# Optimization experiments

Measured on AMD Instinct MI355X. Metric: run time of the kernel, lower is better.

The kernel has to match this reference:

```python
import jax, jax.numpy as jnp
import numpy as np

D_MODEL = 1024
NUM_HEADS = 16
D_K = D_MODEL // NUM_HEADS
THETA = 10000.0
BATCH, SEQ = 2, 2048


def apply_rope(x, token_positions, theta):
    # x: [..., heads, seq, d_k]; interleaved pair rotation
    d = x.shape[-1]
    inv_freq = theta ** (-jnp.arange(0, d, 2, dtype=jnp.float32) / d)  # [d/2]
    ang = token_positions.astype(jnp.float32)[:, None] * inv_freq[None, :]  # [seq, d/2]
    cos, sin = jnp.cos(ang), jnp.sin(ang)  # broadcast over batch/heads
    x_even = x[..., 0::2]
    x_odd = x[..., 1::2]
    out_even = x_even * cos - x_odd * sin
    out_odd = x_even * sin + x_odd * cos
    out = jnp.stack([out_even, out_odd], axis=-1)  # [..., seq, d/2, 2]
    return out.reshape(x.shape)


def setup_inputs() -> dict:
    key = jax.random.key(0)
    ks = jax.random.split(key, 5)
    scale = 1.0 / np.sqrt(D_MODEL)
    return {
        "x": jax.random.normal(ks[0], (BATCH, SEQ, D_MODEL), dtype=jnp.float32),
        "wq": jax.random.normal(ks[1], (D_MODEL, D_MODEL), dtype=jnp.float32) * scale,
        "wk": jax.random.normal(ks[2], (D_MODEL, D_MODEL), dtype=jnp.float32) * scale,
        "wv": jax.random.normal(ks[3], (D_MODEL, D_MODEL), dtype=jnp.float32) * scale,
        "wo": jax.random.normal(ks[4], (D_MODEL, D_MODEL), dtype=jnp.float32) * scale,
        "token_positions": jnp.arange(SEQ, dtype=jnp.int32),
    }


def reference(x, wq, wk, wv, wo, token_positions):
    B, S, _ = x.shape
    # fused-style QKV projections: weight layout is [d_out, d_in]
    xq = jnp.einsum("bsd,kd->bsk", x, wq)
    xk = jnp.einsum("bsd,kd->bsk", x, wk)
    xv = jnp.einsum("bsd,vd->bsv", x, wv)
    # split heads: [b, h, s, d_h]
    def split(t):
        return t.reshape(B, S, NUM_HEADS, D_K).transpose(0, 2, 1, 3)
    xq, xk, xv = split(xq), split(xk), split(xv)
    xq = apply_rope(xq, token_positions, THETA)
    xk = apply_rope(xk, token_positions, THETA)
    scores = jnp.einsum("bhqd,bhkd->bhqk", xq, xk) / jnp.sqrt(jnp.float32(D_K))
    causal = jnp.tril(jnp.ones((S, S), dtype=bool))
    scores = jnp.where(causal, scores, -jnp.inf)
    attn = jax.nn.softmax(scores, axis=-1)
    out = jnp.einsum("bhqk,bhkd->bhqd", attn, xv)
    out = out.transpose(0, 2, 1, 3).reshape(B, S, D_MODEL)  # merge heads
    return jnp.einsum("bsv,dv->bsd", out, wo)
```

## Files before the change

### kernel.cpp

```cpp
#include <hip/hip_runtime.h>

typedef __attribute__((ext_vector_type(8))) short short8;
typedef __attribute__((ext_vector_type(4))) short short4v;
typedef __attribute__((ext_vector_type(4))) float floatx4;

__device__ inline ushort f2b(float f) {
    union { uint i; float f; } c; c.f = f;
    uint i = c.i;
    uint r = (i + 0x7FFFu + ((i >> 16) & 1u)) >> 16;
    return (ushort)r;
}

__device__ __forceinline__ void load_lds16(const ushort* g, ushort* l) {
    __builtin_amdgcn_global_load_lds((const __attribute__((address_space(1))) void*)g,
                                     (__attribute__((address_space(3))) void*)l, 16, 0, 0);
}

__global__ __launch_bounds__(256) void cvt4_k(const float* __restrict__ x,
                                              const float* __restrict__ wq,
                                              const float* __restrict__ wk,
                                              const float* __restrict__ wv,
                                              ushort* __restrict__ xb,
                                              ushort* __restrict__ wqb,
                                              ushort* __restrict__ wkb,
                                              ushort* __restrict__ wvb,
                                              const int* __restrict__ pos,
                                              float2* __restrict__ tab) {
    const int blk = blockIdx.x;
    if (blk >= 3584) {
        const int idx = (blk - 3584) * 256 + threadIdx.x;
        const int s = idx >> 5, fi = idx & 31;
        const float inv = exp2f(-(float)fi * 0.41524101186092557f);
        const float ang = (float)pos[s] * inv;
        float sn, cs;
        sincosf(ang, &sn, &cs);
        tab[idx] = make_float2(cs, sn);
        return;
    }
    const float* in; ushort* out; int base;
    if (blk < 2048)      { in = x;  out = xb;  base = blk; }
    else if (blk < 2560) { in = wq; out = wqb; base = blk - 2048; }
    else if (blk < 3072) { in = wk; out = wkb; base = blk - 2560; }
    else                 { in = wv; out = wvb; base = blk - 3072; }
    const int i = (base * 256 + threadIdx.x) * 8;
    float4 f0 = *(const float4*)(in + i);
    float4 f1 = *(const float4*)(in + i + 4);
    ushort u[8] = {f2b(f0.x), f2b(f0.y), f2b(f0.z), f2b(f0.w),
                   f2b(f1.x), f2b(f1.y), f2b(f1.z), f2b(f1.w)};
    *(uint4*)(out + i) = *(const uint4*)u;
}

template <bool OUTF32, bool BF32>
__device__ __forceinline__ void gemm_body(ushort* As, ushort* Bs,
                                          const ushort* __restrict__ A,
                                          const ushort* __restrict__ Bb,
                                          const float* __restrict__ B32,
                                          void* __restrict__ C,
                                          int N, int m0, int n0,
                                          bool doRope, const float2* __restrict__ tab,
                                          float oscale) {
    const int tid = threadIdx.x;
    const int wave = tid >> 6, lane = tid & 63;
    const int quad = lane >> 4, l16 = lane & 15;
    const int wm = (wave >> 1) * 64, wn = (wave & 1) * 64;

    floatx4 acc[4][4] = {};

    const int cA = tid, cB = tid + 256;
    const int rA = cA >> 2, jgA = ((cA & 3) - (rA >> 1)) & 3;
    const int rB = cB >> 2, jgB = ((cB & 3) - (rB >> 1)) & 3;
    const ushort* gaA = A + (size_t)(m0 + rA) * 1024 + jgA * 8;
    const ushort* gaB = A + (size_t)(m0 + rB) * 1024 + jgB * 8;
    const ushort* gbA = nullptr;
    const ushort* gbB = nullptr;
    const float*  hbA = nullptr;
    const float*  hbB = nullptr;
    if constexpr (!BF32) {
        gbA = Bb + (size_t)(n0 + rA) * 1024 + jgA * 8;
        gbB = Bb + (size_t)(n0 + rB) * 1024 + jgB * 8;
    } else {
        hbA = B32 + (size_t)(n0 + rA) * 1024 + jgA * 8;
        hbB = B32 + (size_t)(n0 + rB) * 1024 + jgB * 8;
    }

    load_lds16(gaA, As + cA * 8);
    load_lds16(gaB, As + cB * 8);
    if constexpr (!BF32) {
        load_lds16(gbA, Bs + cA * 8);
        load_lds16(gbB, Bs + cB * 8);
    } else {
        float4 a0 = *(const float4*)hbA, a1 = *(const float4*)(hbA + 4);
        float4 b0 = *(const float4*)hbB, b1 = *(const float4*)(hbB + 4);
        ushort ua[8] = {f2b(a0.x), f2b(a0.y), f2b(a0.z), f2b(a0.w),
                        f2b(a1.x), f2b(a1.y), f2b(a1.z), f2b(a1.w)};
        ushort ub[8] = {f2b(b0.x), f2b(b0.y), f2b(b0.z), f2b(b0.w),
                        f2b(b1.x), f2b(b1.y), f2b(b1.z), f2b(b1.w)};
        *(uint4*)(Bs + cA * 8) = *(const uint4*)ua;
        *(uint4*)(Bs + cB * 8) = *(const uint4*)ub;
    }
    __syncthreads();

    for (int kt = 0; kt < 32; ++kt) {
        const int cur = kt & 1;
        const int nb = (cur ^ 1) * 4096;
        float4 pa0, pa1, pb0, pb1;
        if (kt + 1 < 32) {
            load_lds16(gaA + (kt + 1) * 32, As + nb + cA * 8);
            load_lds16(gaB + (kt + 1) * 32, As + nb + cB * 8);
            if constexpr (!BF32) {
                load_lds16(gbA + (kt + 1) * 32, Bs + nb + cA * 8);
                load_lds16(gbB + (kt + 1) * 32, Bs + nb + cB * 8);
            } else {
                const float* pA = hbA + (kt + 1) * 32;
                const float* pB = hbB + (kt + 1) * 32;
                pa0 = *(const float4*)pA; pa1 = *(const float4*)(pA + 4);
                pb0 = *(const float4*)pB; pb1 = *(const float4*)(pB + 4);
            }
        }
        const ushort* as = As + cur * 4096;
        const ushort* bs = Bs + cur * 4096;
        short8 af[4], bf[4];
#pragma unroll
        for (int i = 0; i < 4; ++i) {
            const int ra = wm + i * 16 + l16;
            const int rb = wn + i * 16 + l16;
            af[i] = *(const short8*)(as + ra * 32 + (((quad + (ra >> 1)) & 3) << 3));
            bf[i] = *(const short8*)(bs + rb * 32 + (((quad + (rb >> 1)) & 3) << 3));
        }
#pragma unroll
        for (int mi = 0; mi < 4; ++mi)
#pragma unroll
            for (int ni = 0; ni < 4; ++ni)
                acc[mi][ni] = __builtin_amdgcn_mfma_f32_16x16x32_bf16(af[mi], bf[ni], acc[mi][ni], 0, 0, 0);
        if constexpr (BF32) {
            if (kt + 1 < 32) {
                ushort ua[8] = {f2b(pa0.x), f2b(pa0.y), f2b(pa0.z), f2b(pa0.w),
                                f2b(pa1.x), f2b(pa1.y), f2b(pa1.z), f2b(pa1.w)};
                ushort ub[8] = {f2b(pb0.x), f2b(pb0.y), f2b(pb0.z), f2b(pb0.w),
                                f2b(pb1.x), f2b(pb1.y), f2b(pb1.z), f2b(pb1.w)};
                *(uint4*)(Bs + nb + cA * 8) = *(const uint4*)ua;
                *(uint4*)(Bs + nb + cB * 8) = *(const uint4*)ub;
            }
        }
        __syncthreads();
    }
#pragma unroll
    for (int mi = 0; mi < 4; ++mi) {
        const int row = m0 + wm + mi * 16 + quad * 4;
#pragma unroll
        for (int ni = 0; ni < 4; ++ni) {
            const int col = n0 + wn + ni * 16 + l16;
            const int fi = ((wn + ni * 16 + l16) & 63) >> 1;
#pragma unroll
            for (int r = 0; r < 4; ++r) {
                float v = acc[mi][ni][r];
                if (doRope) {
                    const float other = __shfl_xor(v, 1);
                    const float2 cs = tab[((row + r) & 2047) * 32 + fi];
                    v = (col & 1) ? (other * cs.y + v * cs.x) : (v * cs.x - other * cs.y);
                }
                v *= oscale;
                if (OUTF32) ((float*)C)[(size_t)(row + r) * N + col] = v;
                else        ((ushort*)C)[(size_t)(row + r) * N + col] = f2b(v);
            }
        }
    }
}

__global__ __launch_bounds__(256) void gemm_qkv(const ushort* __restrict__ xb,
                                                const ushort* __restrict__ wqb,
                                                const ushort* __restrict__ wkb,
                                                const ushort* __restrict__ wvb,
                                                ushort* __restrict__ q,
                                                ushort* __restrict__ k,
                                                ushort* __restrict__ vt,
                                                const float2* __restrict__ tab) {
    __shared__ __align__(16) ushort As[8192], Bs[8192];
    const int blk = blockIdx.x;
    const int swz = (blk & 7) * 96 + (blk >> 3);
    const int job = swz >> 8, r = swz & 255;
    const ushort *A, *B;
    ushort* C;
    int N, m0, n0;
    bool rope;
    float osc;
    if (job == 0)      { A = xb;  B = wqb; C = q;  N = 1024; m0 = (r >> 3) * 128; n0 = (r & 7) * 128; rope = true;  osc = 0.18033688011112042f; }
    else if (job == 1) { A = xb;  B = wkb; C = k;  N = 1024; m0 = (r >> 3) * 128; n0 = (r & 7) * 128; rope = true;  osc = 1.0f; }
    else               { A = wvb; B = xb;  C = vt; N = 4096; m0 = (r & 7) * 128;  n0 = (r >> 3) * 128; rope = false; osc = 1.0f; }
    gemm_body<false, false>(As, Bs, A, B, nullptr, C, N, m0, n0, rope, tab, osc);
}

__global__ __launch_bounds__(256) void gemm_o(const ushort* __restrict__ A,
                                              const float* __restrict__ wo,
                                              float* __restrict__ C) {
    __shared__ __align__(16) ushort As[8192], Bs[8192];
    const int blk = blockIdx.x;
    const int swz = (blk & 7) * 32 + (blk >> 3);
    const int m = swz >> 3, n = swz & 7;
    gemm_body<true, true>(As, Bs, A, nullptr, wo, C, 1024, m * 128, n * 128, false, nullptr, 1.0f);
}

__global__ __launch_bounds__(256, 4) void attn_k(const ushort* __restrict__ Qg,
                                                 const ushort* __restrict__ Kg,
                                                 const ushort* __restrict__ Vtg,
                                                 ushort* __restrict__ Og) {
    __shared__ __align__(16) ushort Ks[2][4096];
    __shared__ __align__(16) ushort Vs[2][4096];

    const int tid = threadIdx.x;
    const int wave = tid >> 6, lane = tid & 63;
    const int quad = lane >> 4, l16 = lane & 15;
    const int blk = blockIdx.x;
    const int bh = blk & 31;
    const int qt = 31 - (blk >> 5);
    const int b = bh >> 4, h = bh & 15;
    const int bq = b * 2048;
    const int wl = wave * 16 + l16;
    const int nk = qt + 1, dt = nk - 1;

    const int cA = tid, cB = tid + 256;
    const int sA = cA >> 3, jA = ((cA & 7) - sA) & 7;
    const int sB = cB >> 3, jB = ((cB & 7) - sB) & 7;
    const ushort* kgA = Kg + (size_t)(bq + sA) * 1024 + h * 64 + jA * 8;
    const ushort* kgB = Kg + (size_t)(bq + sB) * 1024 + h * 64 + jB * 8;
    const ushort* vgA = Vtg + (size_t)(h * 64 + sA) * 4096 + bq + jA * 8;
    const ushort* vgB = Vtg + (size_t)(h * 64 + sB) * 4096 + bq + jB * 8;

    const int kb0 = l16 * 64 + (((quad + l16) & 7) << 3);
    const int kb1 = l16 * 64 + (((quad + 4 + l16) & 7) << 3);
    int vbs[4];
#pragma unroll
    for (int cb = 0; cb < 4; ++cb)
        vbs[cb] = l16 * 64 + (((cb * 2 + (quad >> 1) + l16) & 7) << 3) + (quad & 1) * 4;

    const ushort* qrow = Qg + (size_t)(bq + qt * 64 + wl) * 1024 + h * 64 + quad * 8;
    const short8 qf0 = *(const short8*)qrow;
    const short8 qf1 = *(const short8*)(qrow + 32);

    floatx4 od[4] = {};
    float l_st = 0.0f;

    load_lds16(kgA, &Ks[0][cA * 8]);
    load_lds16(kgB, &Ks[0][cB * 8]);
    load_lds16(vgA, &Vs[0][cA * 8]);
    load_lds16(vgB, &Vs[0][cB * 8]);
    __syncthreads();

    const ushort* kgA2 = kgA + 65536;
    const ushort* kgB2 = kgB + 65536;
    const ushort* vgA2 = vgA + 64;
    const ushort* vgB2 = vgB + 64;

    auto step = [&](int kt, bool diag, bool pref) {
        const int cur = kt & 1;
        if (pref) {
            const int nxt = cur ^ 1;
            load_lds16(kgA2, &Ks[nxt][cA * 8]);
            load_lds16(kgB2, &Ks[nxt][cB * 8]);
            load_lds16(vgA2, &Vs[nxt][cA * 8]);
            load_lds16(vgB2, &Vs[nxt][cB * 8]);
            kgA2 += 65536; kgB2 += 65536; vgA2 += 64; vgB2 += 64;
        }
        const ushort* kc = &Ks[cur][0];
        const ushort* vc = &Vs[cur][0];

        floatx4 st[4];
        __builtin_amdgcn_s_setprio(1);
#pragma unroll
        for (int cb = 0; cb < 4; ++cb) {
            short8 kf0 = *(const short8*)(kc + kb0 + cb * 1024);
            short8 kf1 = *(const short8*)(kc + kb1 + cb * 1024);
            floatx4 z = {};
            z = __builtin_amdgcn_mfma_f32_16x16x32_bf16(kf0, qf0, z, 0, 0, 0);
            z = __builtin_amdgcn_mfma_f32_16x16x32_bf16(kf1, qf1, z, 0, 0, 0);
            st[cb] = z;
        }
        __builtin_amdgcn_s_setprio(0);

        float pv[4][4];
        float sum = 0.0f;
#pragma unroll
        for (int cb = 0; cb < 4; ++cb) {
            const int scb = cb * 16 + quad * 4;
#pragma unroll
            for (int r = 0; r < 4; ++r) {
                float e = exp2f(st[cb][r]);
                if (diag && (scb + r > wl)) e = 0.0f;
                pv[cb][r] = e;
                sum += e;
            }
        }
        sum += __shfl_xor(sum, 16);
        sum += __shfl_xor(sum, 32);
        l_st += sum;

        short4v pb[4];
#pragma unroll
        for (int cb = 0; cb < 4; ++cb) {
            uint lo_, hi_;
            asm("v_cvt_pk_bf16_f32 %0, %1, %2" : "=v"(lo_) : "v"(pv[cb][0]), "v"(pv[cb][1]));
            asm("v_cvt_pk_bf16_f32 %0, %1, %2" : "=v"(hi_) : "v"(pv[cb][2]), "v"(pv[cb][3]));
            union { uint u[2]; short4v s; } cvu;
            cvu.u[0] = lo_; cvu.u[1] = hi_;
            pb[cb] = cvu.s;
        }

        __builtin_amdgcn_s_setprio(1);
#pragma unroll
        for (int db = 0; db < 4; ++db) {
#pragma unroll
            for (int cb = 0; cb < 4; ++cb) {
                short4v vf = *(const short4v*)(vc + vbs[cb] + db * 1024);
                od[db] = __builtin_amdgcn_mfma_f32_16x16x16bf16_1k(vf, pb[cb], od[db], 0, 0, 0);
            }
        }
        __builtin_amdgcn_s_setprio(0);
        if (pref) __syncthreads();
    };

    for (int kt = 0; kt < dt; ++kt) step(kt, false, true);
    step(dt, true, false);

    const float linv = 1.0f / l_st;
    ushort* orow = Og + (size_t)(bq + qt * 64 + wl) * 1024 + h * 64 + quad * 4;
#pragma unroll
    for (int db = 0; db < 4; ++db) {
        uint2 w;
        w.x = (uint)f2b(od[db][0] * linv) | ((uint)f2b(od[db][1] * linv) << 16);
        w.y = (uint)f2b(od[db][2] * linv) | ((uint)f2b(od[db][3] * linv) << 16);
        *(uint2*)(orow + db * 16) = w;
    }
}

extern "C" void kernel_launch(void* const* d_in, const int* in_sizes, int n_in,
                              void* d_out, int out_size, void* d_ws, size_t ws_size,
                              hipStream_t stream) {
    const float* x  = (const float*)d_in[0];
    const float* wq = (const float*)d_in[1];
    const float* wk = (const float*)d_in[2];
    const float* wv = (const float*)d_in[3];
    const float* wo = (const float*)d_in[4];
    const int* pos  = (const int*)d_in[5];

    const size_t NX = (size_t)4096 * 1024;
    const size_t NW = (size_t)1024 * 1024;

    ushort* q_ws  = (ushort*)d_ws;
    ushort* k_ws  = q_ws + NX;
    ushort* vt_ws = k_ws + NX;
    ushort* o_ws  = vt_ws + NX;
    ushort* xb  = (ushort*)d_out;
    ushort* wqb = xb + NX;
    ushort* wkb = wqb + NW;
    ushort* wvb = wkb + NW;
    float2* tab = (float2*)(wvb + NW);

    cvt4_k<<<dim3(3840), 256, 0, stream>>>(x, wq, wk, wv, xb, wqb, wkb, wvb, pos, tab);
    gemm_qkv<<<dim3(768), 256, 0, stream>>>(xb, wqb, wkb, wvb, q_ws, k_ws, vt_ws, tab);
    attn_k<<<dim3(1024), 256, 0, stream>>>(q_ws, k_ws, vt_ws, o_ws);
    gemm_o<<<dim3(256), 256, 0, stream>>>(o_ws, wo, (float*)d_out);
}
```

Baseline: 203.8 us.

## Switch QKV GEMM and attention to triple-buffered LDS with one barrier per step

Replaces double-buffered LDS staging in the QKV GEMM and the attention kernel with a three-stage ring. Loads run two tiles ahead, and each step uses a vmcnt wait plus a single barrier instead of two __syncthreads. The aim is to hide global-to-LDS latency better and to drop one barrier per iteration. In exchange, LDS use per block goes up by half, attention occupancy is lowered from 4 to 3 blocks, and the output GEMM is split into its own non-templated copy.

```diff
diff --git a/kernel.cpp b/kernel.cpp
--- a/kernel.cpp
+++ b/kernel.cpp
@@ -50,15 +50,13 @@
     *(uint4*)(out + i) = *(const uint4*)u;
 }
 
-template <bool OUTF32, bool BF32>
-__device__ __forceinline__ void gemm_body(ushort* As, ushort* Bs,
-                                          const ushort* __restrict__ A,
-                                          const ushort* __restrict__ Bb,
-                                          const float* __restrict__ B32,
-                                          void* __restrict__ C,
-                                          int N, int m0, int n0,
-                                          bool doRope, const float2* __restrict__ tab,
-                                          float oscale) {
+__device__ __forceinline__ void gemm_body_pipe(ushort* As, ushort* Bs,
+                                               const ushort* __restrict__ A,
+                                               const ushort* __restrict__ B,
+                                               ushort* __restrict__ C,
+                                               int N, int m0, int n0,
+                                               bool doRope, const float2* __restrict__ tab,
+                                               float oscale) {
     const int tid = threadIdx.x;
     const int wave = tid >> 6, lane = tid & 63;
     const int quad = lane >> 4, l16 = lane & 15;
@@ -71,51 +69,32 @@
     const int rB = cB >> 2, jgB = ((cB & 3) - (rB >> 1)) & 3;
     const ushort* gaA = A + (size_t)(m0 + rA) * 1024 + jgA * 8;
     const ushort* gaB = A + (size_t)(m0 + rB) * 1024 + jgB * 8;
-    const ushort* gbA = nullptr;
-    const ushort* gbB = nullptr;
-    const float*  hbA = nullptr;
-    const float*  hbB = nullptr;
-    if constexpr (!BF32) {
-        gbA = Bb + (size_t)(n0 + rA) * 1024 + jgA * 8;
-        gbB = Bb + (size_t)(n0 + rB) * 1024 + jgB * 8;
-    } else {
-        hbA = B32 + (size_t)(n0 + rA) * 1024 + jgA * 8;
-        hbB = B32 + (size_t)(n0 + rB) * 1024 + jgB * 8;
-    }
-
-    load_lds16(gaA, As + cA * 8);
-    load_lds16(gaB, As + cB * 8);
-    if constexpr (!BF32) {
-        load_lds16(gbA, Bs + cA * 8);
-        load_lds16(gbB, Bs + cB * 8);
-    } else {
-        float4 a0 = *(const float4*)hbA, a1 = *(const float4*)(hbA + 4);
-        float4 b0 = *(const float4*)hbB, b1 = *(const float4*)(hbB + 4);
-        ushort ua[8] = {f2b(a0.x), f2b(a0.y), f2b(a0.z), f2b(a0.w),
-                        f2b(a1.x), f2b(a1.y), f2b(a1.z), f2b(a1.w)};
-        ushort ub[8] = {f2b(b0.x), f2b(b0.y), f2b(b0.z), f2b(b0.w),
-                        f2b(b1.x), f2b(b1.y), f2b(b1.z), f2b(b1.w)};
-        *(uint4*)(Bs + cA * 8) = *(const uint4*)ua;
-        *(uint4*)(Bs + cB * 8) = *(const uint4*)ub;
-    }
-    __syncthreads();
-
+    const ushort* gbA = B + (size_t)(n0 + rA) * 1024 + jgA * 8;
+    const ushort* gbB = B + (size_t)(n0 + rB) * 1024 + jgB * 8;
+
+    load_lds16(gaA,      As + cA * 8);
+    load_lds16(gaB,      As + cB * 8);
+    load_lds16(gbA,      Bs + cA * 8);
+    load_lds16(gbB,      Bs + cB * 8);
+    load_lds16(gaA + 32, As + 4096 + cA * 8);
+    load_lds16(gaB + 32, As + 4096 + cB * 8);
+    load_lds16(gbA + 32, Bs + 4096 + cA * 8);
+    load_lds16(gbB + 32, Bs + 4096 + cB * 8);
+
+    int cur = 0;
     for (int kt = 0; kt < 32; ++kt) {
-        const int cur = kt & 1;
-        const int nb = (cur ^ 1) * 4096;
-        float4 pa0, pa1, pb0, pb1;
-        if (kt + 1 < 32) {
-            load_lds16(gaA + (kt + 1) * 32, As + nb + cA * 8);
-            load_lds16(gaB + (kt + 1) * 32, As + nb + cB * 8);
-            if constexpr (!BF32) {
-                load_lds16(gbA + (kt + 1) * 32, Bs + nb + cA * 8);
-                load_lds16(gbB + (kt + 1) * 32, Bs + nb + cB * 8);
-            } else {
-                const float* pA = hbA + (kt + 1) * 32;
-                const float* pB = hbB + (kt + 1) * 32;
-                pa0 = *(const float4*)pA; pa1 = *(const float4*)(pA + 4);
-                pb0 = *(const float4*)pB; pb1 = *(const float4*)(pB + 4);
-            }
+        if (kt < 31) asm volatile("s_waitcnt vmcnt(4)" ::: "memory");
+        else         asm volatile("s_waitcnt vmcnt(0)" ::: "memory");
+        __builtin_amdgcn_s_barrier();
+        __builtin_amdgcn_sched_barrier(0);
+        if (kt + 2 < 32) {
+            const int pf = cur ? cur - 1 : 2;
+            ushort* an = As + pf * 4096;
+            ushort* bn = Bs + pf * 4096;
+            load_lds16(gaA + (kt + 2) * 32, an + cA * 8);
+            load_lds16(gaB + (kt + 2) * 32, an + cB * 8);
+            load_lds16(gbA + (kt + 2) * 32, bn + cA * 8);
+            load_lds16(gbB + (kt + 2) * 32, bn + cB * 8);
         }
         const ushort* as = As + cur * 4096;
         const ushort* bs = Bs + cur * 4096;
@@ -132,17 +111,7 @@
 #pragma unroll
             for (int ni = 0; ni < 4; ++ni)
                 acc[mi][ni] = __builtin_amdgcn_mfma_f32_16x16x32_bf16(af[mi], bf[ni], acc[mi][ni], 0, 0, 0);
-        if constexpr (BF32) {
-            if (kt + 1 < 32) {
-                ushort ua[8] = {f2b(pa0.x), f2b(pa0.y), f2b(pa0.z), f2b(pa0.w),
-                                f2b(pa1.x), f2b(pa1.y), f2b(pa1.z), f2b(pa1.w)};
-                ushort ub[8] = {f2b(pb0.x), f2b(pb0.y), f2b(pb0.z), f2b(pb0.w),
-                                f2b(pb1.x), f2b(pb1.y), f2b(pb1.z), f2b(pb1.w)};
-                *(uint4*)(Bs + nb + cA * 8) = *(const uint4*)ua;
-                *(uint4*)(Bs + nb + cB * 8) = *(const uint4*)ub;
-            }
-        }
-        __syncthreads();
+        cur = (cur == 2) ? 0 : cur + 1;
     }
 #pragma unroll
     for (int mi = 0; mi < 4; ++mi) {
@@ -160,8 +129,7 @@
                     v = (col & 1) ? (other * cs.y + v * cs.x) : (v * cs.x - other * cs.y);
                 }
                 v *= oscale;
-                if (OUTF32) ((float*)C)[(size_t)(row + r) * N + col] = v;
-                else        ((ushort*)C)[(size_t)(row + r) * N + col] = f2b(v);
+                ((ushort*)C)[(size_t)(row + r) * N + col] = f2b(v);
             }
         }
     }
@@ -175,7 +143,7 @@
                                                 ushort* __restrict__ k,
                                                 ushort* __restrict__ vt,
                                                 const float2* __restrict__ tab) {
-    __shared__ __align__(16) ushort As[8192], Bs[8192];
+    __shared__ __align__(16) ushort As[12288], Bs[12288];
     const int blk = blockIdx.x;
     const int swz = (blk & 7) * 96 + (blk >> 3);
     const int job = swz >> 8, r = swz & 255;
@@ -187,7 +155,7 @@
     if (job == 0)      { A = xb;  B = wqb; C = q;  N = 1024; m0 = (r >> 3) * 128; n0 = (r & 7) * 128; rope = true;  osc = 0.18033688011112042f; }
     else if (job == 1) { A = xb;  B = wkb; C = k;  N = 1024; m0 = (r >> 3) * 128; n0 = (r & 7) * 128; rope = true;  osc = 1.0f; }
     else               { A = wvb; B = xb;  C = vt; N = 4096; m0 = (r & 7) * 128;  n0 = (r >> 3) * 128; rope = false; osc = 1.0f; }
-    gemm_body<false, false>(As, Bs, A, B, nullptr, C, N, m0, n0, rope, tab, osc);
+    gemm_body_pipe(As, Bs, A, B, C, N, m0, n0, rope, tab, osc);
 }
 
 __global__ __launch_bounds__(256) void gemm_o(const ushort* __restrict__ A,
@@ -196,16 +164,93 @@
     __shared__ __align__(16) ushort As[8192], Bs[8192];
     const int blk = blockIdx.x;
     const int swz = (blk & 7) * 32 + (blk >> 3);
-    const int m = swz >> 3, n = swz & 7;
-    gemm_body<true, true>(As, Bs, A, nullptr, wo, C, 1024, m * 128, n * 128, false, nullptr, 1.0f);
-}
-
-__global__ __launch_bounds__(256, 4) void attn_k(const ushort* __restrict__ Qg,
+    const int m0 = (swz >> 3) * 128, n0 = (swz & 7) * 128;
+
+    const int tid = threadIdx.x;
+    const int wave = tid >> 6, lane = tid & 63;
+    const int quad = lane >> 4, l16 = lane & 15;
+    const int wm = (wave >> 1) * 64, wn = (wave & 1) * 64;
+
+    floatx4 acc[4][4] = {};
+
+    const int cA = tid, cB = tid + 256;
+    const int rA = cA >> 2, jgA = ((cA & 3) - (rA >> 1)) & 3;
+    const int rB = cB >> 2, jgB = ((cB & 3) - (rB >> 1)) & 3;
+    const ushort* gaA = A + (size_t)(m0 + rA) * 1024 + jgA * 8;
+    const ushort* gaB = A + (size_t)(m0 + rB) * 1024 + jgB * 8;
+    const float*  hbA = wo + (size_t)(n0 + rA) * 1024 + jgA * 8;
+    const float*  hbB = wo + (size_t)(n0 + rB) * 1024 + jgB * 8;
+
+    load_lds16(gaA, As + cA * 8);
+    load_lds16(gaB, As + cB * 8);
+    {
+        float4 a0 = *(const float4*)hbA, a1 = *(const float4*)(hbA + 4);
+        float4 b0 = *(const float4*)hbB, b1 = *(const float4*)(hbB + 4);
+        ushort ua[8] = {f2b(a0.x), f2b(a0.y), f2b(a0.z), f2b(a0.w),
+                        f2b(a1.x), f2b(a1.y), f2b(a1.z), f2b(a1.w)};
+        ushort ub[8] = {f2b(b0.x), f2b(b0.y), f2b(b0.z), f2b(b0.w),
+                        f2b(b1.x), f2b(b1.y), f2b(b1.z), f2b(b1.w)};
+        *(uint4*)(Bs + cA * 8) = *(const uint4*)ua;
+        *(uint4*)(Bs + cB * 8) = *(const uint4*)ub;
+    }
+    __syncthreads();
+
+    for (int kt = 0; kt < 32; ++kt) {
+        const int cur = kt & 1;
+        const int nb = (cur ^ 1) * 4096;
+        float4 pa0, pa1, pb0, pb1;
+        if (kt + 1 < 32) {
+            load_lds16(gaA + (kt + 1) * 32, As + nb + cA * 8);
+            load_lds16(gaB + (kt + 1) * 32, As + nb + cB * 8);
+            const float* pA = hbA + (kt + 1) * 32;
+            const float* pB = hbB + (kt + 1) * 32;
+            pa0 = *(const float4*)pA; pa1 = *(const float4*)(pA + 4);
+            pb0 = *(const float4*)pB; pb1 = *(const float4*)(pB + 4);
+        }
+        const ushort* as = As + cur * 4096;
+        const ushort* bs = Bs + cur * 4096;
+        short8 af[4], bf[4];
+#pragma unroll
+        for (int i = 0; i < 4; ++i) {
+            const int ra = wm + i * 16 + l16;
+            const int rb = wn + i * 16 + l16;
+            af[i] = *(const short8*)(as + ra * 32 + (((quad + (ra >> 1)) & 3) << 3));
+            bf[i] = *(const short8*)(bs + rb * 32 + (((quad + (rb >> 1)) & 3) << 3));
+        }
+#pragma unroll
+        for (int mi = 0; mi < 4; ++mi)
+#pragma unroll
+            for (int ni = 0; ni < 4; ++ni)
+                acc[mi][ni] = __builtin_amdgcn_mfma_f32_16x16x32_bf16(af[mi], bf[ni], acc[mi][ni], 0, 0, 0);
+        if (kt + 1 < 32) {
+            ushort ua[8] = {f2b(pa0.x), f2b(pa0.y), f2b(pa0.z), f2b(pa0.w),
+                            f2b(pa1.x), f2b(pa1.y), f2b(pa1.z), f2b(pa1.w)};
+            ushort ub[8] = {f2b(pb0.x), f2b(pb0.y), f2b(pb0.z), f2b(pb0.w),
+                            f2b(pb1.x), f2b(pb1.y), f2b(pb1.z), f2b(pb1.w)};
+            *(uint4*)(Bs + nb + cA * 8) = *(const uint4*)ua;
+            *(uint4*)(Bs + nb + cB * 8) = *(const uint4*)ub;
+        }
+        __syncthreads();
+    }
+#pragma unroll
+    for (int mi = 0; mi < 4; ++mi) {
+        const int row = m0 + wm + mi * 16 + quad * 4;
+#pragma unroll
+        for (int ni = 0; ni < 4; ++ni) {
+            const int col = n0 + wn + ni * 16 + l16;
+#pragma unroll
+            for (int r = 0; r < 4; ++r)
+                C[(size_t)(row + r) * 1024 + col] = acc[mi][ni][r];
+        }
+    }
+}
+
+__global__ __launch_bounds__(256, 3) void attn_k(const ushort* __restrict__ Qg,
                                                  const ushort* __restrict__ Kg,
                                                  const ushort* __restrict__ Vtg,
                                                  ushort* __restrict__ Og) {
-    __shared__ __align__(16) ushort Ks[2][4096];
-    __shared__ __align__(16) ushort Vs[2][4096];
+    __shared__ __align__(16) ushort Ks[3][4096];
+    __shared__ __align__(16) ushort Vs[3][4096];
 
     const int tid = threadIdx.x;
     const int wave = tid >> 6, lane = tid & 63;
@@ -244,25 +289,20 @@
     load_lds16(kgB, &Ks[0][cB * 8]);
     load_lds16(vgA, &Vs[0][cA * 8]);
     load_lds16(vgB, &Vs[0][cB * 8]);
-    __syncthreads();
-
-    const ushort* kgA2 = kgA + 65536;
-    const ushort* kgB2 = kgB + 65536;
-    const ushort* vgA2 = vgA + 64;
-    const ushort* vgB2 = vgB + 64;
-
-    auto step = [&](int kt, bool diag, bool pref) {
-        const int cur = kt & 1;
-        if (pref) {
-            const int nxt = cur ^ 1;
-            load_lds16(kgA2, &Ks[nxt][cA * 8]);
-            load_lds16(kgB2, &Ks[nxt][cB * 8]);
-            load_lds16(vgA2, &Vs[nxt][cA * 8]);
-            load_lds16(vgB2, &Vs[nxt][cB * 8]);
-            kgA2 += 65536; kgB2 += 65536; vgA2 += 64; vgB2 += 64;
-        }
-        const ushort* kc = &Ks[cur][0];
-        const ushort* vc = &Vs[cur][0];
+    if (nk > 1) {
+        load_lds16(kgA + 65536, &Ks[1][cA * 8]);
+        load_lds16(kgB + 65536, &Ks[1][cB * 8]);
+        load_lds16(vgA + 64,    &Vs[1][cA * 8]);
+        load_lds16(vgB + 64,    &Vs[1][cB * 8]);
+    }
+    const ushort* kgA2 = kgA + 2 * 65536;
+    const ushort* kgB2 = kgB + 2 * 65536;
+    const ushort* vgA2 = vgA + 2 * 64;
+    const ushort* vgB2 = vgB + 2 * 64;
+
+    auto compute = [&](int buf, bool diag) {
+        const ushort* kc = &Ks[buf][0];
+        const ushort* vc = &Vs[buf][0];
 
         floatx4 st[4];
         __builtin_amdgcn_s_setprio(1);
@@ -315,11 +355,28 @@
             }
         }
         __builtin_amdgcn_s_setprio(0);
-        if (pref) __syncthreads();
     };
 
-    for (int kt = 0; kt < dt; ++kt) step(kt, false, true);
-    step(dt, true, false);
+    int cur = 0;
+    for (int kt = 0; kt < dt; ++kt) {
+        asm volatile("s_waitcnt vmcnt(4)" ::: "memory");
+        __builtin_amdgcn_s_barrier();
+        __builtin_amdgcn_sched_barrier(0);
+        if (kt + 2 < nk) {
+            const int pf = cur ? cur - 1 : 2;
+            load_lds16(kgA2, &Ks[pf][cA * 8]);
+            load_lds16(kgB2, &Ks[pf][cB * 8]);
+            load_lds16(vgA2, &Vs[pf][cA * 8]);
+            load_lds16(vgB2, &Vs[pf][cB * 8]);
+            kgA2 += 65536; kgB2 += 65536; vgA2 += 64; vgB2 += 64;
+        }
+        compute(cur, false);
+        cur = (cur == 2) ? 0 : cur + 1;
+    }
+    asm volatile("s_waitcnt vmcnt(0)" ::: "memory");
+    __builtin_amdgcn_s_barrier();
+    __builtin_amdgcn_sched_barrier(0);
+    compute(cur, true);
 
     const float linv = 1.0f / l_st;
     ushort* orow = Og + (size_t)(bq + qt * 64 + wl) * 1024 + h * 64 + quad * 4;
```

Result: slower. 228.5 us (+12.1%).
